# Kernel optimization log

Hardware: AMD Instinct MI355X
Metric: run time of the kernel (lower is better)

The kernel has to match this reference:

```python
import jax, jax.numpy as jnp
import numpy as np

CUTOFF = 10.0


def _forward(query_points, codes, grid_points, eW1, eb1, eW2, eb2, cW, cb, fcW, fcb, nW1, nb1, nW2, nb2, edge_index):
    B, N, _ = query_points.shape
    G = grid_points.shape[0]
    C = codes.shape[-1]
    n_pts = B * N
    num_nodes = n_pts + B * G
    qp = query_points.reshape(-1, 3)
    gc = jnp.broadcast_to(grid_points[None], (B, G, 3)).reshape(-1, 3)
    x = jnp.concatenate([qp, gc], axis=0)                      # [num_nodes, 3]
    h = jnp.concatenate([jnp.zeros((n_pts, C), qp.dtype), codes.reshape(-1, C)], axis=0)
    row, col = edge_index[0], edge_index[1]                    # row = grid (source), col = query (target)
    ones = jnp.ones((edge_index.shape[1],), x.dtype)
    denom = jnp.maximum(jax.ops.segment_sum(ones, col, num_segments=num_nodes), 1.0)[:, None]

    def layer(x, h, We1, be1, We2, be2, Wc, bc, Wn1, bn1, Wn2, bn2, out_x_dim):
        rel = x[row] - x[col]                                  # [E, 3]
        dist = jnp.linalg.norm(rel, axis=-1, keepdims=True)    # [E, 1]
        m = jax.nn.silu(jnp.concatenate([h[row], h[col], dist], axis=-1) @ We1 + be1)
        m = jax.nn.silu(m @ We2 + be2)                         # [E, H]
        d = dist[:, 0]
        Cm = 0.5 * (jnp.cos(d * jnp.pi / CUTOFF) + 1.0) * (d <= CUTOFF)
        m = m * Cm[:, None]
        coef = m @ Wc + bc                                     # [E, out_x_dim]
        dirn = rel / (dist + 1e-8)
        if out_x_dim == 1:
            cmsg = coef * dirn                                 # [E, 3]
            dx = jax.ops.segment_sum(cmsg, col, num_segments=num_nodes) / denom
            x_new = x + dx
        else:
            cmsg = (coef[:, :, None] * dirn[:, None, :]).reshape(coef.shape[0], -1)  # [E, T*3]
            dx = (jax.ops.segment_sum(cmsg, col, num_segments=num_nodes) / denom).reshape(num_nodes, out_x_dim, 3)
            x_new = x[:, None, :] + dx                         # [num_nodes, T, 3]
        m_aggr = jax.ops.segment_sum(m, col, num_segments=num_nodes) / denom
        h_delta = jax.nn.silu(jnp.concatenate([h, m_aggr], axis=-1) @ Wn1 + bn1) @ Wn2 + bn2
        return x_new, h + h_delta

    for i in range(3):
        x, h = layer(x, h, eW1[i], eb1[i], eW2[i], eb2[i], cW[i], cb[i], nW1[i], nb1[i], nW2[i], nb2[i], 1)
    T = fcb.shape[0]
    x_f, _ = layer(x, h, eW1[3], eb1[3], eW2[3], eb2[3], fcW, fcb, nW1[3], nb1[3], nW2[3], nb2[3], T)
    pred = x_f[:n_pts].reshape(B, N, T, 3)
    return pred - query_points.reshape(B, N, 3)[:, :, None, :]


def setup_inputs() -> dict:
    key = jax.random.key(0)
    B, N, Gs, Cd, H, T, deg = 8, 2048, 8, 128, 128, 5, 16
    G = Gs ** 3
    n_pts = B * N
    E = n_pts * deg
    ks = jax.random.split(key, 12)
    c1 = (jnp.arange(Gs, dtype=jnp.float32) - (Gs - 1) / 2.0) * 2.0   # anchor_spacing = 2.0, centered
    gx, gy, gz = jnp.meshgrid(c1, c1, c1, indexing='ij')
    grid_points = jnp.stack([gx, gy, gz], -1).reshape(-1, 3)
    query_points = jax.random.uniform(ks[0], (B, N, 3), minval=-7.0, maxval=7.0)
    codes = jax.random.normal(ks[1], (B, G, Cd), dtype=jnp.float32)
    q = jnp.repeat(jnp.arange(n_pts, dtype=jnp.int32), deg)
    gl = jax.random.randint(ks[2], (E,), 0, G, dtype=jnp.int32)
    row = n_pts + (q // N) * G + gl                                   # grid node (global idx), same batch as query
    edge_index = jnp.stack([row, q], axis=0)
    def lin(k, fi, sh):
        return jax.random.normal(k, sh, dtype=jnp.float32) / jnp.sqrt(jnp.float32(fi))
    eW1 = lin(ks[3], 2 * Cd + 1, (4, 2 * Cd + 1, H)); eb1 = jnp.zeros((4, H))
    eW2 = lin(ks[4], H, (4, H, H)); eb2 = jnp.zeros((4, H))
    cW = lin(ks[5], H, (3, H, 1)); cb = jnp.zeros((3, 1))
    fcW = lin(ks[6], H, (H, T)); fcb = jnp.zeros((T,))
    nW1 = lin(ks[7], Cd + H, (4, Cd + H, H)); nb1 = jnp.zeros((4, H))
    nW2 = lin(ks[8], H, (4, H, Cd)); nb2 = jnp.zeros((4, Cd))
    return {"query_points": query_points, "codes": codes, "grid_points": grid_points,
            "eW1": eW1, "eb1": eb1, "eW2": eW2, "eb2": eb2,
            "cW": cW, "cb": cb, "fcW": fcW, "fcb": fcb,
            "nW1": nW1, "nb1": nb1, "nW2": nW2, "nb2": nb2,
            "edge_index": edge_index}


def reference(query_points, codes, grid_points, eW1, eb1, eW2, eb2, cW, cb, fcW, fcb, nW1, nb1, nW2, nb2, edge_index):
    return _forward(query_points, codes, grid_points, eW1, eb1, eW2, eb2, cW, cb, fcW, fcb, nW1, nb1, nW2, nb2, edge_index)
```

## Files before the change

kernel.cpp:

```cpp
#include <hip/hip_runtime.h>
#include <hip/hip_bf16.h>

typedef unsigned short u16;
typedef unsigned int u32;
typedef __attribute__((ext_vector_type(8))) short short8;
typedef __attribute__((ext_vector_type(4))) short shortx4;
typedef __attribute__((ext_vector_type(4))) float floatx4;

#define N_PTS 16384
#define N_GRID 4096
#define GPTS 512
#define HD 128
#define DEG 16
#define QB 16
#define EB 256
#define EBLK (N_PTS / QB)

__device__ __forceinline__ float silu_f(float x) {
    return x * __builtin_amdgcn_rcpf(1.0f + __expf(-x));
}
__device__ __forceinline__ short f2bf(float x) { return (short)__bfloat16_as_ushort(__float2bfloat16(x)); }

__global__ void k_fillf(float* out, float v, int n) {
    int i = blockIdx.x * blockDim.x + threadIdx.x;
    if (i < n) out[i] = v;
}

__global__ void k_prepAll(const float* __restrict__ eW2, const float* __restrict__ nW1,
                          const float* __restrict__ nW2, const float* __restrict__ eW1,
                          short* __restrict__ wsT, short* __restrict__ nW1T,
                          short* __restrict__ nW2T, short* __restrict__ W1midT,
                          short* __restrict__ W1topT) {
    int idx = blockIdx.x * blockDim.x + threadIdx.x;
    if (idx < 65536) {
        int l = idx >> 14, rem = idx & 16383, f = rem >> 7, k = rem & 127;
        wsT[idx] = f2bf(eW2[l * 16384 + k * HD + f]);
        return;
    }
    idx -= 65536;
    if (idx < 3 * 32768) {
        int l = idx >> 15, r = idx & 32767, f = r >> 8, k = r & 255;
        nW1T[idx] = f2bf(nW1[l * 32768 + k * 128 + f]);
    } else if (idx < 3 * 32768 + 3 * 16384) {
        int j = idx - 3 * 32768;
        int l = j >> 14, r = j & 16383, f = r >> 7, k = r & 127;
        nW2T[j] = f2bf(nW2[l * 16384 + k * 128 + f]);
    } else if (idx < 3 * 32768 + 6 * 16384) {
        int j = idx - 3 * 32768 - 3 * 16384;
        int p = j >> 14, r = j & 16383, f = r >> 7, k = r & 127;
        W1midT[j] = f2bf(eW1[(p + 1) * 257 * 128 + (128 + k) * 128 + f]);
    } else if (idx < 3 * 32768 + 6 * 16384 + 4 * 16384) {
        int j = idx - 3 * 32768 - 6 * 16384;
        int l = j >> 14, r = j & 16383, f = r >> 7, k = r & 127;
        W1topT[j] = f2bf(eW1[l * 257 * 128 + k * 128 + f]);
    }
}

__device__ __forceinline__ void stageB(short* Bb, const short* src, int rowF4, int colF4, int tid) {
#pragma unroll
    for (int s = 0; s < 8; s++) {
        int idx = s * 256 + tid;
        int f = idx >> 4, c4 = idx & 15;
        float4 v = ((const float4*)src)[f * rowF4 + colF4 + c4];
        *(float4*)((char*)Bb + ((idx * 16) ^ ((f & 7) << 4))) = v;
    }
}

__device__ __forceinline__ void stageB512(short* Bb, const short* src, int rowF4, int colF4, int tid) {
#pragma unroll
    for (int s = 0; s < 4; s++) {
        int idx = s * 512 + tid;
        int f = idx >> 4, c4 = idx & 15;
        float4 v = ((const float4*)src)[f * rowF4 + colF4 + c4];
        *(float4*)((char*)Bb + ((idx * 16) ^ ((f & 7) << 4))) = v;
    }
}

__device__ __forceinline__ void nb_gemm(const short* X1, const short* Bb, floatx4* acc,
                                        int rowbase, int kOff, int quad, int c, int swz) {
#pragma unroll
    for (int ks = 0; ks < 4; ks++) {
        short8 a = *(const short8*)((const char*)X1 + rowbase + (((kOff + ks * 32 + quad * 8) * 2) ^ swz));
#pragma unroll
        for (int n = 0; n < 8; n++) {
            short8 b = *(const short8*)((const char*)Bb + ((((n * 16 + c) << 8) + (ks * 32 + quad * 8) * 2) ^ swz));
            acc[n] = __builtin_amdgcn_mfma_f32_16x16x32_bf16(a, b, acc[n], 0, 0, 0);
        }
    }
}

__device__ __forceinline__ void gemm16(const short* X, const short* Bb, floatx4& acc,
                                       int kOffX, int wid, int quad, int c, int swz) {
#pragma unroll
    for (int ks = 0; ks < 4; ks++) {
        int k = ks * 32 + quad * 8;
        short8 a = *(const short8*)((const char*)X + ((c * 512 + (kOffX + k) * 2) ^ swz));
        short8 b = *(const short8*)((const char*)Bb + ((((wid * 16 + c) << 8) + k * 2) ^ swz));
        acc = __builtin_amdgcn_mfma_f32_16x16x32_bf16(a, b, acc, 0, 0, 0);
    }
}

__global__ __launch_bounds__(256) void k_gm(
    const float* __restrict__ codes, float* __restrict__ Agall,
    const short* __restrict__ W1topT, const float* __restrict__ eb1,
    const short* __restrict__ nW1T, const float* __restrict__ nb1,
    const short* __restrict__ nW2T, const float* __restrict__ nb2) {
    __shared__ float hgF[64 * 128];
    __shared__ short X[64 * 128];
    __shared__ short Bb[128 * 128];
    int tid = threadIdx.x;
    int n0 = blockIdx.x * 64;
    int wid = tid >> 6, lane = tid & 63, quad = lane >> 4, c = lane & 15;
    const int swz = (c & 7) << 4;
    int rowbase = (wid * 16 + c) * 256;

    {
        int q = tid >> 2, part = tid & 3;
        const float* src = &codes[(n0 + q) * HD + part * 32];
        int wswz = (q & 7) << 4;
#pragma unroll
        for (int i = 0; i < 4; i++) {
            float4 a = ((const float4*)src)[2 * i];
            float4 b = ((const float4*)src)[2 * i + 1];
            *(float4*)&hgF[q * 128 + part * 32 + i * 8] = a;
            *(float4*)&hgF[q * 128 + part * 32 + i * 8 + 4] = b;
            short8 v;
            v[0] = f2bf(a.x); v[1] = f2bf(a.y); v[2] = f2bf(a.z); v[3] = f2bf(a.w);
            v[4] = f2bf(b.x); v[5] = f2bf(b.y); v[6] = f2bf(b.z); v[7] = f2bf(b.w);
            *(short8*)((char*)X + ((q * 256 + part * 64 + i * 16) ^ wswz)) = v;
        }
    }

    for (int L = 0; L < 4; L++) {
        stageB(Bb, W1topT + L * 16384, 16, 0, tid);
        __syncthreads();
        floatx4 acc[8];
#pragma unroll
        for (int n = 0; n < 8; n++) acc[n] = (floatx4)0.f;
        nb_gemm(X, Bb, acc, rowbase, 0, quad, c, swz);
        float* Ag = Agall + (size_t)L * (N_GRID * HD);
#pragma unroll
        for (int n = 0; n < 8; n++) {
            int f = n * 16 + c;
            float bv = eb1[L * 128 + f];
#pragma unroll
            for (int r = 0; r < 4; r++)
                Ag[(n0 + wid * 16 + quad * 4 + r) * HD + f] = acc[n][r] + bv;
        }
        if (L == 3) break;

        __syncthreads();
        stageB(Bb, nW1T + L * 32768, 32, 0, tid);
        __syncthreads();
#pragma unroll
        for (int n = 0; n < 8; n++) acc[n] = (floatx4)0.f;
        nb_gemm(X, Bb, acc, rowbase, 0, quad, c, swz);
        __syncthreads();
#pragma unroll
        for (int n = 0; n < 8; n++) {
            int f = n * 16 + c;
            float b1v = nb1[L * 128 + f];
#pragma unroll
            for (int r = 0; r < 4; r++) {
                int rq = wid * 16 + quad * 4 + r;
                *(short*)((char*)X + ((rq * 256 + f * 2) ^ ((rq & 7) << 4))) =
                    f2bf(silu_f(acc[n][r] + b1v));
            }
        }
        stageB(Bb, nW2T + L * 16384, 16, 0, tid);
        __syncthreads();
#pragma unroll
        for (int n = 0; n < 8; n++) acc[n] = (floatx4)0.f;
        nb_gemm(X, Bb, acc, rowbase, 0, quad, c, swz);
        __syncthreads();
#pragma unroll
        for (int n = 0; n < 8; n++) {
            int f = n * 16 + c;
            float b2v2 = nb2[L * 128 + f];
#pragma unroll
            for (int r = 0; r < 4; r++) {
                int rq = wid * 16 + quad * 4 + r;
                hgF[rq * 128 + f] += acc[n][r] + b2v2;
            }
        }
        __syncthreads();
        {
            int q = tid >> 2, part = tid & 3;
            int wswz = (q & 7) << 4;
#pragma unroll
            for (int i = 0; i < 4; i++) {
                float4 a = *(const float4*)&hgF[q * 128 + part * 32 + i * 8];
                float4 b = *(const float4*)&hgF[q * 128 + part * 32 + i * 8 + 4];
                short8 v;
                v[0] = f2bf(a.x); v[1] = f2bf(a.y); v[2] = f2bf(a.z); v[3] = f2bf(a.w);
                v[4] = f2bf(b.x); v[5] = f2bf(b.y); v[6] = f2bf(b.z); v[7] = f2bf(b.w);
                *(short8*)((char*)X + ((q * 256 + part * 64 + i * 16) ^ wswz)) = v;
            }
        }
    }
}

template <int OUTT, bool FIN>
__device__ __forceinline__ void edge_layer(
    int L, int q0, int tid, float4& hreg,
    float* misc, float* xs, int* sgi, short* Xn, float* BqF, short* lwsT,
    const float* __restrict__ Agall, const float* __restrict__ eW1,
    const short* __restrict__ wsT,
    const float* __restrict__ eb2all, const float* __restrict__ cWall,
    const float* __restrict__ cball,
    const float* __restrict__ fcW, const float* __restrict__ fcb,
    const float* __restrict__ gridp, const float* __restrict__ qp,
    float* __restrict__ out,
    const float* __restrict__ nb1all, const float* __restrict__ nb2all,
    const short* __restrict__ nW1T, const short* __restrict__ nW2T,
    const short* __restrict__ W1midT) {

    float* sdist = misc;
    float* scm   = misc + 256;
    float* sdir  = misc + 512;
    float* scoef = misc + 1280;
    float* delta = misc;

    int wid = tid >> 6, lane = tid & 63, quad = lane >> 4, c = lane & 15;
    const int swz = (c & 7) << 4;
    const float* Ag = Agall + (size_t)L * (N_GRID * HD);
    const short* wsTL = wsT + L * 16384;
    const float* wdrow = eW1 + L * 257 * 128 + 256 * 128;
    const float* b2v = eb2all + L * 128;
    const float* Wc = FIN ? fcW : (cWall + L * 128);
    const float* cbp = FIN ? fcb : (cball + L);

    {
        const float4* src = (const float4*)wsTL;
#pragma unroll
        for (int s = 0; s < 4; s++) {
            int idx = s * 512 + tid;
            int byte = idx << 4;
            int sw = byte ^ (((byte >> 8) & 7) << 4);
            *(float4*)((char*)lwsT + sw) = src[idx];
        }
    }
    if (tid < EB) {
        int e = tid, q = e >> 4;
        int gi = sgi[e];
        int gl = gi & (GPTS - 1);
        float r0 = gridp[gl * 3 + 0] - xs[q * 3 + 0];
        float r1 = gridp[gl * 3 + 1] - xs[q * 3 + 1];
        float r2 = gridp[gl * 3 + 2] - xs[q * 3 + 2];
        float dist = sqrtf(r0 * r0 + r1 * r1 + r2 * r2);
        float inv = 1.0f / (dist + 1e-8f);
        sdist[e] = dist;
        sdir[0 * EB + e] = r0 * inv;
        sdir[1 * EB + e] = r1 * inv;
        sdir[2 * EB + e] = r2 * inv;
        float cw = 0.5f * (__cosf(dist * 0.31415926535897931f) + 1.0f);
        scm[e] = (dist <= 10.0f) ? cw : 0.0f;
    }
    __syncthreads();

    int gi_[2]; float dist_[2];
#pragma unroll
    for (int mi = 0; mi < 2; mi++) {
        int e = (wid * 2 + mi) * 16 + c;
        gi_[mi] = sgi[e];
        dist_[mi] = sdist[e];
    }

    floatx4 acc[2][8];
#pragma unroll
    for (int mi = 0; mi < 2; mi++)
#pragma unroll
        for (int n = 0; n < 8; n++) acc[mi][n] = (floatx4)0.f;

#pragma unroll
    for (int ch = 0; ch < 4; ch++) {
        int kb = ch * 32 + quad * 8;
        float4 wd0 = *(const float4*)(wdrow + kb);
        float4 wd1 = *(const float4*)(wdrow + kb + 4);
        short8 afr[2];
#pragma unroll
        for (int mi = 0; mi < 2; mi++) {
            int q = wid * 2 + mi;
            float dist = dist_[mi];
            const float4* ap = (const float4*)(Ag + gi_[mi] * HD + kb);
            float4 a0 = ap[0], a1 = ap[1];
            const float4* bp4 = (const float4*)(BqF + q * HD + kb);
            float4 b0 = bp4[0], b1 = bp4[1];
            short8 v;
            v[0] = f2bf(silu_f(a0.x + b0.x + dist * wd0.x));
            v[1] = f2bf(silu_f(a0.y + b0.y + dist * wd0.y));
            v[2] = f2bf(silu_f(a0.z + b0.z + dist * wd0.z));
            v[3] = f2bf(silu_f(a0.w + b0.w + dist * wd0.w));
            v[4] = f2bf(silu_f(a1.x + b1.x + dist * wd1.x));
            v[5] = f2bf(silu_f(a1.y + b1.y + dist * wd1.y));
            v[6] = f2bf(silu_f(a1.z + b1.z + dist * wd1.z));
            v[7] = f2bf(silu_f(a1.w + b1.w + dist * wd1.w));
            afr[mi] = v;
        }
#pragma unroll
        for (int n = 0; n < 8; n++) {
            int byte = ((n * 16 + c) << 8) + (kb << 1);
            short8 bfr = *(const short8*)((const char*)lwsT + (byte ^ swz));
            acc[0][n] = __builtin_amdgcn_mfma_f32_16x16x32_bf16(afr[0], bfr, acc[0][n], 0, 0, 0);
            acc[1][n] = __builtin_amdgcn_mfma_f32_16x16x32_bf16(afr[1], bfr, acc[1][n], 0, 0, 0);
        }
    }
    __syncthreads();

#pragma unroll
    for (int mi = 0; mi < 2; mi++) {
        int q = wid * 2 + mi;
        int ebase = q * 16;
        float cmr[4];
#pragma unroll
        for (int r = 0; r < 4; r++) cmr[r] = scm[ebase + quad * 4 + r];
        float apc[4][OUTT];
#pragma unroll
        for (int r = 0; r < 4; r++)
#pragma unroll
            for (int t = 0; t < OUTT; t++) apc[r][t] = 0.f;
#pragma unroll
        for (int n = 0; n < 8; n++) {
            int f = n * 16 + c;
            float be2v = b2v[f];
            float wcv[OUTT];
            if (FIN) {
#pragma unroll
                for (int t = 0; t < OUTT; t++) wcv[t] = Wc[f * 5 + t];
            } else {
                wcv[0] = Wc[f];
            }
            float cs = 0.f;
#pragma unroll
            for (int r = 0; r < 4; r++) {
                float v = silu_f(acc[mi][n][r] + be2v) * cmr[r];
                cs += v;
#pragma unroll
                for (int t = 0; t < OUTT; t++) apc[r][t] += v * wcv[t];
            }
            cs += __shfl_xor(cs, 16, 64);
            cs += __shfl_xor(cs, 32, 64);
            if (!FIN && lane < 16)
                *(short*)((char*)Xn + ((q * 512 + (128 + f) * 2) ^ ((q & 7) << 4))) =
                    f2bf(cs * 0.0625f);
        }
#pragma unroll
        for (int t = 0; t < OUTT; t++) {
#pragma unroll
            for (int r = 0; r < 4; r++) {
                float v = apc[r][t];
                v += __shfl_xor(v, 1, 64);
                v += __shfl_xor(v, 2, 64);
                v += __shfl_xor(v, 4, 64);
                v += __shfl_xor(v, 8, 64);
                if (c == 0) scoef[(ebase + quad * 4 + r) * OUTT + t] = v;
            }
        }
    }
    __syncthreads();

    if (tid < QB * 3 * OUTT) {
        int qq = tid / (3 * OUTT), rem = tid % (3 * OUTT), t = rem / 3, c2 = rem % 3;
        float cbv = cbp[t];
        float s = 0.f;
#pragma unroll 4
        for (int r = 0; r < 16; r++) {
            int ee = qq * 16 + r;
            s += (scoef[ee * OUTT + t] + cbv) * sdir[c2 * EB + ee];
        }
        float dd = s * 0.0625f;
        if (FIN) out[(q0 + qq) * 15 + t * 3 + c2] = xs[qq * 3 + c2] + dd - qp[(q0 + qq) * 3 + c2];
        else xs[qq * 3 + c2] = xs[qq * 3 + c2] + dd;
    }
    if (FIN) return;

    {
        int q = tid >> 5, f0 = (tid & 31) * 4;
        shortx4 v;
        v[0] = f2bf(hreg.x); v[1] = f2bf(hreg.y); v[2] = f2bf(hreg.z); v[3] = f2bf(hreg.w);
        *(shortx4*)((char*)Xn + ((q * 512 + f0 * 2) ^ ((q & 7) << 4))) = v;
    }
    stageB512(lwsT, nW1T + L * 32768, 32, 0, tid);
    __syncthreads();

    floatx4 acc1 = (floatx4)0.f;
    gemm16(Xn, lwsT, acc1, 0, wid, quad, c, swz);
    __syncthreads();
    stageB512(lwsT, nW1T + L * 32768, 32, 16, tid);
    __syncthreads();
    gemm16(Xn, lwsT, acc1, 128, wid, quad, c, swz);
    __syncthreads();

    {
        int f = wid * 16 + c;
        float b1v = nb1all[L * 128 + f];
#pragma unroll
        for (int r = 0; r < 4; r++) {
            int q = quad * 4 + r;
            *(short*)((char*)Xn + ((q * 512 + (128 + f) * 2) ^ ((q & 7) << 4))) =
                f2bf(silu_f(acc1[r] + b1v));
        }
    }
    stageB512(lwsT, nW2T + L * 16384, 16, 0, tid);
    __syncthreads();

    floatx4 acc2 = (floatx4)0.f;
    gemm16(Xn, lwsT, acc2, 128, wid, quad, c, swz);
    __syncthreads();

    {
        int f = wid * 16 + c;
        float b2 = nb2all[L * 128 + f];
#pragma unroll
        for (int r = 0; r < 4; r++)
            delta[(quad * 4 + r) * 128 + f] = acc2[r] + b2;
    }
    stageB512(lwsT, W1midT + L * 16384, 16, 0, tid);
    __syncthreads();

    {
        int q = tid >> 5, f0 = (tid & 31) * 4;
        hreg.x += delta[q * 128 + f0 + 0];
        hreg.y += delta[q * 128 + f0 + 1];
        hreg.z += delta[q * 128 + f0 + 2];
        hreg.w += delta[q * 128 + f0 + 3];
        shortx4 v;
        v[0] = f2bf(hreg.x); v[1] = f2bf(hreg.y); v[2] = f2bf(hreg.z); v[3] = f2bf(hreg.w);
        *(shortx4*)((char*)Xn + ((q * 512 + f0 * 2) ^ ((q & 7) << 4))) = v;
    }
    __syncthreads();

    floatx4 acc3 = (floatx4)0.f;
    gemm16(Xn, lwsT, acc3, 0, wid, quad, c, swz);
    __syncthreads();
    {
        int f = wid * 16 + c;
#pragma unroll
        for (int r = 0; r < 4; r++)
            BqF[(quad * 4 + r) * 128 + f] = acc3[r];
    }
    __syncthreads();
}

__global__ __launch_bounds__(512, 2) void k_mega(
    const float* __restrict__ Agall, const float* __restrict__ eW1,
    const short* __restrict__ wsT,
    const float* __restrict__ eb2, const float* __restrict__ cW,
    const float* __restrict__ cb,
    const float* __restrict__ fcW, const float* __restrict__ fcb,
    const int* __restrict__ erow, const float* __restrict__ gridp,
    const float* __restrict__ qp, float* __restrict__ out,
    const float* __restrict__ nb1, const float* __restrict__ nb2,
    const short* __restrict__ nW1T, const short* __restrict__ nW2T,
    const short* __restrict__ W1midT) {
    __shared__ float misc[2560];
    __shared__ float xs[48];
    __shared__ int sgi[256];
    __shared__ union { short xn[16 * 256]; float bq[16 * 128]; } XB;
    __shared__ short lwsT[HD * HD];
    int tid = threadIdx.x;
    int sb = (blockIdx.x & 7) * (EBLK / 8) + (blockIdx.x >> 3);
    int q0 = sb * QB;

    if (tid < QB * 3) xs[tid] = qp[q0 * 3 + tid];
    if (tid < EB) sgi[tid] = erow[q0 * DEG + tid] - N_PTS;
    for (int i = tid; i < 16 * 128; i += 512) XB.bq[i] = 0.0f;
    float4 hreg = make_float4(0.f, 0.f, 0.f, 0.f);
    __syncthreads();

    for (int L = 0; L < 3; L++)
        edge_layer<1, false>(L, q0, tid, hreg, misc, xs, sgi, XB.xn, XB.bq, lwsT,
                             Agall, eW1, wsT, eb2, cW, cb, fcW, fcb, gridp, qp, out,
                             nb1, nb2, nW1T, nW2T, W1midT);
    edge_layer<5, true>(3, q0, tid, hreg, misc, xs, sgi, XB.xn, XB.bq, lwsT,
                        Agall, eW1, wsT, eb2, cW, cb, fcW, fcb, gridp, qp, out,
                        nb1, nb2, nW1T, nW2T, W1midT);
}

extern "C" void kernel_launch(void* const* d_in, const int* in_sizes, int n_in,
                              void* d_out, int out_size, void* d_ws, size_t ws_size,
                              hipStream_t stream) {
    float* out = (float*)d_out;
    int fill_blocks = (out_size + 255) / 256;

    static const int exp_sz[16] = { 49152, 524288, 1536, 131584, 512, 65536, 512, 384,
                                    3, 640, 5, 131072, 512, 65536, 512, 524288 };
    bool ok = (n_in == 16);
    for (int i = 0; ok && i < 16; i++) if (in_sizes[i] != exp_sz[i]) ok = false;
    if (!ok || ws_size < (size_t)40 * 1024 * 1024) {
        k_fillf<<<fill_blocks, 256, 0, stream>>>(out, 777.0f, out_size);
        return;
    }

    const float* qp    = (const float*)d_in[0];
    const float* codes = (const float*)d_in[1];
    const float* gridp = (const float*)d_in[2];
    const float* eW1   = (const float*)d_in[3];
    const float* eb1   = (const float*)d_in[4];
    const float* eW2   = (const float*)d_in[5];
    const float* eb2   = (const float*)d_in[6];
    const float* cW    = (const float*)d_in[7];
    const float* cb    = (const float*)d_in[8];
    const float* fcW   = (const float*)d_in[9];
    const float* fcb   = (const float*)d_in[10];
    const float* nW1   = (const float*)d_in[11];
    const float* nb1   = (const float*)d_in[12];
    const float* nW2   = (const float*)d_in[13];
    const float* nb2   = (const float*)d_in[14];
    const int*   erow  = (const int*)d_in[15];

    float* ws = (float*)d_ws;
    float* Agall = ws;  ws += 4 * N_GRID * HD;
    short* wsT    = (short*)ws;
    short* nW1T   = wsT + 65536;
    short* nW2T   = nW1T + 98304;
    short* W1midT = nW2T + 49152;
    short* W1topT = W1midT + 49152;

    k_prepAll<<<(65536 + 3 * 32768 + 6 * 16384 + 4 * 16384 + 255) / 256, 256, 0, stream>>>(
        eW2, nW1, nW2, eW1, wsT, nW1T, nW2T, W1midT, W1topT);

    k_gm<<<N_GRID / 64, 256, 0, stream>>>(codes, Agall, W1topT, eb1,
                                          nW1T, nb1, nW2T, nb2);

    k_mega<<<EBLK, 512, 0, stream>>>(
        Agall, eW1, wsT, eb2, cW, cb, fcW, fcb, erow, gridp, qp, out,
        nb1, nb2, nW1T, nW2T, W1midT);
}
```

Before: 346.2 us.

## Shrink grid-node GEMM tiles to 16 rows and raise k_mega occupancy hint

k_gm now processes 16 grid nodes per block instead of 64, so it launches four times as many blocks (256 instead of 64) and fills more CUs. Each wave now computes two 16-column output tiles for the shared 16 rows instead of eight tiles for its own rows. In exchange, each block restages the full 128x128 weight matrices, so weight traffic per node rises. Separately, k_mega's launch bounds hint changes from 2 to 3 blocks per CU, which may force register spilling.

```diff
diff --git a/kernel.cpp b/kernel.cpp
--- a/kernel.cpp
+++ b/kernel.cpp
@@ -105,97 +105,114 @@
     const short* __restrict__ W1topT, const float* __restrict__ eb1,
     const short* __restrict__ nW1T, const float* __restrict__ nb1,
     const short* __restrict__ nW2T, const float* __restrict__ nb2) {
-    __shared__ float hgF[64 * 128];
-    __shared__ short X[64 * 128];
+    __shared__ float hgF[16 * 128];
+    __shared__ short X[16 * 128];
     __shared__ short Bb[128 * 128];
     int tid = threadIdx.x;
-    int n0 = blockIdx.x * 64;
+    int n0 = blockIdx.x * 16;
     int wid = tid >> 6, lane = tid & 63, quad = lane >> 4, c = lane & 15;
     const int swz = (c & 7) << 4;
-    int rowbase = (wid * 16 + c) * 256;
-
-    {
-        int q = tid >> 2, part = tid & 3;
-        const float* src = &codes[(n0 + q) * HD + part * 32];
-        int wswz = (q & 7) << 4;
-#pragma unroll
-        for (int i = 0; i < 4; i++) {
-            float4 a = ((const float4*)src)[2 * i];
-            float4 b = ((const float4*)src)[2 * i + 1];
-            *(float4*)&hgF[q * 128 + part * 32 + i * 8] = a;
-            *(float4*)&hgF[q * 128 + part * 32 + i * 8 + 4] = b;
+
+    {
+        int q = tid >> 4, part = tid & 15;
+        const float* src = &codes[(n0 + q) * HD + part * 8];
+        float4 a = ((const float4*)src)[0];
+        float4 b = ((const float4*)src)[1];
+        *(float4*)&hgF[q * 128 + part * 8] = a;
+        *(float4*)&hgF[q * 128 + part * 8 + 4] = b;
+        short8 v;
+        v[0] = f2bf(a.x); v[1] = f2bf(a.y); v[2] = f2bf(a.z); v[3] = f2bf(a.w);
+        v[4] = f2bf(b.x); v[5] = f2bf(b.y); v[6] = f2bf(b.z); v[7] = f2bf(b.w);
+        *(short8*)((char*)X + ((q * 256 + part * 16) ^ ((q & 7) << 4))) = v;
+    }
+
+    for (int L = 0; L < 4; L++) {
+        stageB(Bb, W1topT + L * 16384, 16, 0, tid);
+        __syncthreads();
+        floatx4 acc[2];
+        acc[0] = (floatx4)0.f; acc[1] = (floatx4)0.f;
+#pragma unroll
+        for (int ks = 0; ks < 4; ks++) {
+            int k = ks * 32 + quad * 8;
+            short8 a = *(const short8*)((const char*)X + ((c * 256 + k * 2) ^ swz));
+#pragma unroll
+            for (int j = 0; j < 2; j++) {
+                int n = wid * 2 + j;
+                short8 b = *(const short8*)((const char*)Bb + ((((n * 16 + c) << 8) + k * 2) ^ swz));
+                acc[j] = __builtin_amdgcn_mfma_f32_16x16x32_bf16(a, b, acc[j], 0, 0, 0);
+            }
+        }
+        float* Ag = Agall + (size_t)L * (N_GRID * HD);
+#pragma unroll
+        for (int j = 0; j < 2; j++) {
+            int f = (wid * 2 + j) * 16 + c;
+            float bv = eb1[L * 128 + f];
+#pragma unroll
+            for (int r = 0; r < 4; r++)
+                Ag[(n0 + quad * 4 + r) * HD + f] = acc[j][r] + bv;
+        }
+        if (L == 3) break;
+
+        __syncthreads();
+        stageB(Bb, nW1T + L * 32768, 32, 0, tid);
+        __syncthreads();
+        floatx4 a2[2];
+        a2[0] = (floatx4)0.f; a2[1] = (floatx4)0.f;
+#pragma unroll
+        for (int ks = 0; ks < 4; ks++) {
+            int k = ks * 32 + quad * 8;
+            short8 a = *(const short8*)((const char*)X + ((c * 256 + k * 2) ^ swz));
+#pragma unroll
+            for (int j = 0; j < 2; j++) {
+                int n = wid * 2 + j;
+                short8 b = *(const short8*)((const char*)Bb + ((((n * 16 + c) << 8) + k * 2) ^ swz));
+                a2[j] = __builtin_amdgcn_mfma_f32_16x16x32_bf16(a, b, a2[j], 0, 0, 0);
+            }
+        }
+        __syncthreads();
+#pragma unroll
+        for (int j = 0; j < 2; j++) {
+            int f = (wid * 2 + j) * 16 + c;
+            float b1v = nb1[L * 128 + f];
+#pragma unroll
+            for (int r = 0; r < 4; r++) {
+                int row = quad * 4 + r;
+                *(short*)((char*)X + ((row * 256 + f * 2) ^ ((row & 7) << 4))) =
+                    f2bf(silu_f(a2[j][r] + b1v));
+            }
+        }
+        stageB(Bb, nW2T + L * 16384, 16, 0, tid);
+        __syncthreads();
+        floatx4 a3[2];
+        a3[0] = (floatx4)0.f; a3[1] = (floatx4)0.f;
+#pragma unroll
+        for (int ks = 0; ks < 4; ks++) {
+            int k = ks * 32 + quad * 8;
+            short8 a = *(const short8*)((const char*)X + ((c * 256 + k * 2) ^ swz));
+#pragma unroll
+            for (int j = 0; j < 2; j++) {
+                int n = wid * 2 + j;
+                short8 b = *(const short8*)((const char*)Bb + ((((n * 16 + c) << 8) + k * 2) ^ swz));
+                a3[j] = __builtin_amdgcn_mfma_f32_16x16x32_bf16(a, b, a3[j], 0, 0, 0);
+            }
+        }
+#pragma unroll
+        for (int j = 0; j < 2; j++) {
+            int f = (wid * 2 + j) * 16 + c;
+            float b2v2 = nb2[L * 128 + f];
+#pragma unroll
+            for (int r = 0; r < 4; r++)
+                hgF[(quad * 4 + r) * 128 + f] += a3[j][r] + b2v2;
+        }
+        __syncthreads();
+        {
+            int q = tid >> 4, part = tid & 15;
+            float4 a = *(const float4*)&hgF[q * 128 + part * 8];
+            float4 b = *(const float4*)&hgF[q * 128 + part * 8 + 4];
             short8 v;
             v[0] = f2bf(a.x); v[1] = f2bf(a.y); v[2] = f2bf(a.z); v[3] = f2bf(a.w);
             v[4] = f2bf(b.x); v[5] = f2bf(b.y); v[6] = f2bf(b.z); v[7] = f2bf(b.w);
-            *(short8*)((char*)X + ((q * 256 + part * 64 + i * 16) ^ wswz)) = v;
-        }
-    }
-
-    for (int L = 0; L < 4; L++) {
-        stageB(Bb, W1topT + L * 16384, 16, 0, tid);
-        __syncthreads();
-        floatx4 acc[8];
-#pragma unroll
-        for (int n = 0; n < 8; n++) acc[n] = (floatx4)0.f;
-        nb_gemm(X, Bb, acc, rowbase, 0, quad, c, swz);
-        float* Ag = Agall + (size_t)L * (N_GRID * HD);
-#pragma unroll
-        for (int n = 0; n < 8; n++) {
-            int f = n * 16 + c;
-            float bv = eb1[L * 128 + f];
-#pragma unroll
-            for (int r = 0; r < 4; r++)
-                Ag[(n0 + wid * 16 + quad * 4 + r) * HD + f] = acc[n][r] + bv;
-        }
-        if (L == 3) break;
-
-        __syncthreads();
-        stageB(Bb, nW1T + L * 32768, 32, 0, tid);
-        __syncthreads();
-#pragma unroll
-        for (int n = 0; n < 8; n++) acc[n] = (floatx4)0.f;
-        nb_gemm(X, Bb, acc, rowbase, 0, quad, c, swz);
-        __syncthreads();
-#pragma unroll
-        for (int n = 0; n < 8; n++) {
-            int f = n * 16 + c;
-            float b1v = nb1[L * 128 + f];
-#pragma unroll
-            for (int r = 0; r < 4; r++) {
-                int rq = wid * 16 + quad * 4 + r;
-                *(short*)((char*)X + ((rq * 256 + f * 2) ^ ((rq & 7) << 4))) =
-                    f2bf(silu_f(acc[n][r] + b1v));
-            }
-        }
-        stageB(Bb, nW2T + L * 16384, 16, 0, tid);
-        __syncthreads();
-#pragma unroll
-        for (int n = 0; n < 8; n++) acc[n] = (floatx4)0.f;
-        nb_gemm(X, Bb, acc, rowbase, 0, quad, c, swz);
-        __syncthreads();
-#pragma unroll
-        for (int n = 0; n < 8; n++) {
-            int f = n * 16 + c;
-            float b2v2 = nb2[L * 128 + f];
-#pragma unroll
-            for (int r = 0; r < 4; r++) {
-                int rq = wid * 16 + quad * 4 + r;
-                hgF[rq * 128 + f] += acc[n][r] + b2v2;
-            }
-        }
-        __syncthreads();
-        {
-            int q = tid >> 2, part = tid & 3;
-            int wswz = (q & 7) << 4;
-#pragma unroll
-            for (int i = 0; i < 4; i++) {
-                float4 a = *(const float4*)&hgF[q * 128 + part * 32 + i * 8];
-                float4 b = *(const float4*)&hgF[q * 128 + part * 32 + i * 8 + 4];
-                short8 v;
-                v[0] = f2bf(a.x); v[1] = f2bf(a.y); v[2] = f2bf(a.z); v[3] = f2bf(a.w);
-                v[4] = f2bf(b.x); v[5] = f2bf(b.y); v[6] = f2bf(b.z); v[7] = f2bf(b.w);
-                *(short8*)((char*)X + ((q * 256 + part * 64 + i * 16) ^ wswz)) = v;
-            }
+            *(short8*)((char*)X + ((q * 256 + part * 16) ^ ((q & 7) << 4))) = v;
         }
     }
 }
@@ -442,7 +459,7 @@
     __syncthreads();
 }
 
-__global__ __launch_bounds__(512, 2) void k_mega(
+__global__ __launch_bounds__(512, 3) void k_mega(
     const float* __restrict__ Agall, const float* __restrict__ eW1,
     const short* __restrict__ wsT,
     const float* __restrict__ eb2, const float* __restrict__ cW,
@@ -520,7 +537,7 @@
     k_prepAll<<<(65536 + 3 * 32768 + 6 * 16384 + 4 * 16384 + 255) / 256, 256, 0, stream>>>(
         eW2, nW1, nW2, eW1, wsT, nW1T, nW2T, W1midT, W1topT);
 
-    k_gm<<<N_GRID / 64, 256, 0, stream>>>(codes, Agall, W1topT, eb1,
+    k_gm<<<N_GRID / 16, 256, 0, stream>>>(codes, Agall, W1topT, eb1,
                                           nW1T, nb1, nW2T, nb2);
 
     k_mega<<<EBLK, 512, 0, stream>>>(
```

Result: slower. 483.2 us (+39.6%).
